# Kernel tuning notes

Hardware: AMD Instinct MI355X
Metric: run time of the kernel (lower is better)

Reference implementation:

```python
import jax, jax.numpy as jnp
import numpy as np

B, NPG, F, DEG = 512, 512, 255, 32   # graphs, nodes-per-graph, feat dim, avg degree
N = B * NPG
E = N * DEG
RATIO = 0.5
K = int(np.ceil(RATIO * NPG))        # nodes kept per graph (static)


def setup_inputs() -> dict:
    key = jax.random.key(0)
    k1, k2, k3, k4, k5 = jax.random.split(key, 5)
    out = jax.random.normal(k1, (N, F), jnp.float32)
    z = jax.random.randint(k2, (N,), 0, 101)  # z == 100 marks virtual nodes
    # random edges strictly within each graph (block-contiguous node ids)
    local = jax.random.randint(k3, (2, B, NPG * DEG), 0, NPG)
    offs = (jnp.arange(B) * NPG)[None, :, None]
    edge_index = (local + offs).reshape(2, E)
    batch = jnp.repeat(jnp.arange(B), NPG)
    W = jax.random.normal(k4, (F + 1, 1), jnp.float32) * (1.0 / np.sqrt(F + 1))
    b = jnp.zeros((1,), jnp.float32)
    edge_attr = jax.random.normal(k5, (E, 1), jnp.float32)  # carried but unused by SAGPool scoring
    return dict(out=out, z=z, edge_index=edge_index, batch=batch, W=W, b=b,
                edge_attr=edge_attr)


def gcn_score(x, edge_index, W, b):
    """GCNConv(F+1 -> 1) with self-loops and symmetric normalization."""
    n = x.shape[0]
    h = (x @ W)[:, 0]  # [N] since out_channels == 1
    row, col = edge_index[0], edge_index[1]
    loop = jnp.arange(n)
    row = jnp.concatenate([row, loop])
    col = jnp.concatenate([col, loop])
    deg = jax.ops.segment_sum(jnp.ones_like(col, x.dtype), col, num_segments=n)
    dinv = jnp.where(deg > 0, jax.lax.rsqrt(deg), 0.0)
    norm = dinv[row] * dinv[col]  # deg^-1/2 * deg^-1/2 per edge
    agg = jax.ops.segment_sum(norm * h[row], col, num_segments=n)
    return agg + b[0]


def reference(out, z, edge_index, batch, W, b, edge_attr):
    # concat real/virtual bit
    real = (z != 100).astype(out.dtype)[:, None]
    x = jnp.concatenate([out, real], axis=-1)          # [N, F+1]
    # SAGPooling: score nodes, tanh nonlinearity
    score = jnp.tanh(gcn_score(x, edge_index, W, b))   # [N]
    # per-graph top-k (uniform graph size -> static-shape top_k)
    sv, si = jax.lax.top_k(score.reshape(B, NPG), K)   # [B, K]
    perm = (si + (jnp.arange(B) * NPG)[:, None]).reshape(-1)  # global node ids
    xp = x[perm] * sv.reshape(-1)[:, None]             # gated selected nodes [B*K, F+1]
    # global_mean_pool over pooled batch (k nodes per graph)
    return xp.reshape(B, K, F + 1).mean(axis=1)        # [B, F+1]
```

## Files before the change

### kernel.cpp

```cpp
#include <hip/hip_runtime.h>
#include <math.h>

#define NPG     512
#define B_GR    512
#define FDIM    255
#define DEG     32
#define EPG     (NPG * DEG)
#define N_NODES (B_GR * NPG)
#define E_TOT   (N_NODES * DEG)
#define K_KEEP  256

#define CH_NODES 32
#define CH_F4    ((CH_NODES * FDIM) / 4)
#define NCHUNK   (NPG / CH_NODES)

__global__ __launch_bounds__(1024) void k_fused(const float* __restrict__ feat,
                                                const int*   __restrict__ z,
                                                const int*   __restrict__ ei,
                                                const float* __restrict__ W,
                                                const float* __restrict__ bias,
                                                float*       __restrict__ outp) {
    __shared__ __align__(16) char stagebuf[32768];
    __shared__ float Wl[256];
    __shared__ float h_l[NPG];
    __shared__ float dinv_l[NPG];
    __shared__ float agg[NPG];
    __shared__ float score[NPG];
    __shared__ float realb[NPG];
    __shared__ int   deg[NPG];
    __shared__ int   rank2[2][NPG];
    __shared__ int   selidx[K_KEEP];
    __shared__ float selsc[K_KEEP];
    __shared__ float red[3][256];
    __shared__ int   cnt;

    const int g     = blockIdx.x;
    const int tid   = threadIdx.x;
    const int nbase = g * NPG;

    if (tid < 256) Wl[tid] = W[tid];
    if (tid < NPG) {
        realb[tid] = (z[nbase + tid] != 100) ? 1.f : 0.f;
        deg[tid]   = 1;
        agg[tid]   = 0.f;
    }
    if (tid == 0) cnt = 0;
    __syncthreads();

    {
        float4*      stage4 = (float4*)stagebuf;
        const float* stage  = (const float*)stagebuf;
        const int    wave   = tid >> 6;
        const int    lane   = tid & 63;
        const float4* src   = (const float4*)(feat + (size_t)nbase * FDIM);

        for (int ch = 0; ch < NCHUNK; ++ch) {
            stage4[tid] = src[ch * CH_F4 + tid];
            const int idx2 = 1024 + tid;
            if (idx2 < CH_F4) stage4[idx2] = src[ch * CH_F4 + idx2];
            __syncthreads();
#pragma unroll
            for (int k = 0; k < 2; ++k) {
                const int node = wave * 2 + k;
                const float* row = stage + node * FDIM;
                float acc = (lane == 0) ? realb[ch * CH_NODES + node] * Wl[FDIM] : 0.f;
                acc = fmaf(row[lane],       Wl[lane],       acc);
                acc = fmaf(row[lane + 64],  Wl[lane + 64],  acc);
                acc = fmaf(row[lane + 128], Wl[lane + 128], acc);
                if (lane < 63)
                    acc = fmaf(row[lane + 192], Wl[lane + 192], acc);
#pragma unroll
                for (int off = 32; off; off >>= 1)
                    acc += __shfl_down(acc, off, 64);
                if (lane == 0) h_l[ch * CH_NODES + node] = acc;
            }
            __syncthreads();
        }
    }

    {
        ushort4*    cc4   = (ushort4*)stagebuf;
        const int4* colp4 = (const int4*)(ei + (size_t)E_TOT + (size_t)g * EPG);
        const int4* rowp4 = (const int4*)(ei + (size_t)g * EPG);

#pragma unroll
        for (int it = 0; it < 4; ++it) {
            const int  idx = it * 1024 + tid;
            const int4 c4  = colp4[idx];
            ushort4 u;
            u.x = (unsigned short)(c4.x - nbase);
            u.y = (unsigned short)(c4.y - nbase);
            u.z = (unsigned short)(c4.z - nbase);
            u.w = (unsigned short)(c4.w - nbase);
            cc4[idx] = u;
            atomicAdd(&deg[u.x], 1);
            atomicAdd(&deg[u.y], 1);
            atomicAdd(&deg[u.z], 1);
            atomicAdd(&deg[u.w], 1);
        }
        __syncthreads();

        if (tid < NPG)
            dinv_l[tid] = (float)(1.0 / sqrt((double)deg[tid]));
        __syncthreads();

#pragma unroll
        for (int it = 0; it < 4; ++it) {
            const int     idx = it * 1024 + tid;
            const int4    r4  = rowp4[idx];
            const ushort4 u   = cc4[idx];
            int r;
            r = r4.x - nbase; atomicAdd(&agg[u.x], dinv_l[r] * dinv_l[u.x] * h_l[r]);
            r = r4.y - nbase; atomicAdd(&agg[u.y], dinv_l[r] * dinv_l[u.y] * h_l[r]);
            r = r4.z - nbase; atomicAdd(&agg[u.z], dinv_l[r] * dinv_l[u.z] * h_l[r]);
            r = r4.w - nbase; atomicAdd(&agg[u.w], dinv_l[r] * dinv_l[u.w] * h_l[r]);
        }
        __syncthreads();
    }

    if (tid < NPG)
        score[tid] = tanhf(agg[tid] + dinv_l[tid] * dinv_l[tid] * h_l[tid] + bias[0]);
    __syncthreads();

    {
        const int   node = tid & (NPG - 1);
        const int   half = tid >> 9;
        const float sc   = score[node];
        const int   j0   = half * 256;
        int part = 0;
        for (int i = 0; i < 256; ++i) {
            const int   j  = j0 + i;
            const float sj = score[j];
            part += (sj > sc) || (sj == sc && j < node);
        }
        rank2[half][node] = part;
    }
    __syncthreads();

    if (tid < NPG) {
        const int rank = rank2[0][tid] + rank2[1][tid];
        if (rank < K_KEEP) {
            const int slot = atomicAdd(&cnt, 1);
            selidx[slot] = tid;
            selsc[slot]  = score[tid];
        }
    }
    __syncthreads();

    {
        const int f = tid & 255;
        const int q = tid >> 8;
        float acc = 0.f;
        if (f < FDIM) {
            const float* fb = feat + (size_t)nbase * FDIM + f;
#pragma unroll 8
            for (int s = q; s < K_KEEP; s += 4)
                acc = fmaf(selsc[s], fb[(size_t)selidx[s] * FDIM], acc);
        } else {
#pragma unroll 8
            for (int s = q; s < K_KEEP; s += 4)
                acc = fmaf(selsc[s], realb[selidx[s]], acc);
        }
        if (q) red[q - 1][f] = acc;
        __syncthreads();
        if (q == 0)
            outp[(size_t)g * 256 + f] =
                (acc + red[0][f] + red[1][f] + red[2][f]) * (1.f / K_KEEP);
    }
}

extern "C" void kernel_launch(void* const* d_in, const int* in_sizes, int n_in,
                              void* d_out, int out_size, void* d_ws, size_t ws_size,
                              hipStream_t stream) {
    const float* feat = (const float*)d_in[0];
    const int*   z    = (const int*)  d_in[1];
    const int*   ei   = (const int*)  d_in[2];
    const float* W    = (const float*)d_in[4];
    const float* bias = (const float*)d_in[5];
    float* outp = (float*)d_out;

    k_fused<<<B_GR, 1024, 0, stream>>>(feat, z, ei, W, bias, outp);
}
```

Before: 128.7 us.

## Double-buffer feature staging with direct global-to-LDS loads and vectorize rank scan

Replaces the register-staged feature copy with global_load_lds DMA into two LDS buffers of 16 nodes each, prefetching the next chunk while the current chunk's dot products run. One barrier per chunk replaces two, and the W values are hoisted into registers. The rank computation now reads scores as float4 with an unrolled loop. The trade-offs are more loop iterations with smaller chunks, and reliance on the 16-byte LDS DMA builtin and manual waitcnt handling.

```diff
diff --git a/kernel.cpp b/kernel.cpp
--- a/kernel.cpp
+++ b/kernel.cpp
@@ -10,9 +10,16 @@
 #define E_TOT   (N_NODES * DEG)
 #define K_KEEP  256
 
-#define CH_NODES 32
-#define CH_F4    ((CH_NODES * FDIM) / 4)
-#define NCHUNK   (NPG / CH_NODES)
+#define CH_NODES 16
+#define CH_FLOATS (CH_NODES * FDIM)
+#define CH_F4     (CH_FLOATS / 4)
+#define NCHUNK    (NPG / CH_NODES)
+
+__device__ __forceinline__ void lds_dma16(const void* g, void* l) {
+    __builtin_amdgcn_global_load_lds(
+        (const __attribute__((address_space(1))) unsigned int*)g,
+        (__attribute__((address_space(3))) unsigned int*)l, 16, 0, 0);
+}
 
 __global__ __launch_bounds__(1024) void k_fused(const float* __restrict__ feat,
                                                 const int*   __restrict__ z,
@@ -20,12 +27,12 @@
                                                 const float* __restrict__ W,
                                                 const float* __restrict__ bias,
                                                 float*       __restrict__ outp) {
-    __shared__ __align__(16) char stagebuf[32768];
-    __shared__ float Wl[256];
+    __shared__ __align__(16) float stage[2][CH_FLOATS];
+    __shared__ __align__(16) float Wl[256];
+    __shared__ __align__(16) float score[NPG];
     __shared__ float h_l[NPG];
     __shared__ float dinv_l[NPG];
     __shared__ float agg[NPG];
-    __shared__ float score[NPG];
     __shared__ float realb[NPG];
     __shared__ int   deg[NPG];
     __shared__ int   rank2[2][NPG];
@@ -37,6 +44,8 @@
     const int g     = blockIdx.x;
     const int tid   = threadIdx.x;
     const int nbase = g * NPG;
+    const int lane  = tid & 63;
+    const int wave  = tid >> 6;
 
     if (tid < 256) Wl[tid] = W[tid];
     if (tid < NPG) {
@@ -48,38 +57,47 @@
     __syncthreads();
 
     {
-        float4*      stage4 = (float4*)stagebuf;
-        const float* stage  = (const float*)stagebuf;
-        const int    wave   = tid >> 6;
-        const int    lane   = tid & 63;
-        const float4* src   = (const float4*)(feat + (size_t)nbase * FDIM);
+        const float w0   = Wl[lane];
+        const float w64  = Wl[lane + 64];
+        const float w128 = Wl[lane + 128];
+        const float w192 = (lane < 63) ? Wl[lane + 192] : 0.f;
+        const float w255 = Wl[FDIM];
+        const char* srcb = (const char*)(feat + (size_t)nbase * FDIM);
+
+        if (tid < CH_F4)
+            lds_dma16(srcb + (size_t)tid * 16, (char*)stage[0] + (size_t)tid * 16);
+        asm volatile("s_waitcnt vmcnt(0)" ::: "memory");
+        __builtin_amdgcn_s_barrier();
+        __builtin_amdgcn_sched_barrier(0);
 
         for (int ch = 0; ch < NCHUNK; ++ch) {
-            stage4[tid] = src[ch * CH_F4 + tid];
-            const int idx2 = 1024 + tid;
-            if (idx2 < CH_F4) stage4[idx2] = src[ch * CH_F4 + idx2];
-            __syncthreads();
+            const float* cur = stage[ch & 1];
+            float*       nxt = (float*)stage[(ch & 1) ^ 1];
+            if (ch + 1 < NCHUNK && tid < CH_F4)
+                lds_dma16(srcb + (size_t)(ch + 1) * 16320 + (size_t)tid * 16,
+                          (char*)nxt + (size_t)tid * 16);
+
+            const float* row = cur + wave * FDIM;
+            const float  rb  = realb[ch * CH_NODES + wave];
+            float acc = (lane == 0) ? rb * w255 : 0.f;
+            acc = fmaf(row[lane],       w0,   acc);
+            acc = fmaf(row[lane + 64],  w64,  acc);
+            acc = fmaf(row[lane + 128], w128, acc);
+            if (lane < 63)
+                acc = fmaf(row[lane + 192], w192, acc);
 #pragma unroll
-            for (int k = 0; k < 2; ++k) {
-                const int node = wave * 2 + k;
-                const float* row = stage + node * FDIM;
-                float acc = (lane == 0) ? realb[ch * CH_NODES + node] * Wl[FDIM] : 0.f;
-                acc = fmaf(row[lane],       Wl[lane],       acc);
-                acc = fmaf(row[lane + 64],  Wl[lane + 64],  acc);
-                acc = fmaf(row[lane + 128], Wl[lane + 128], acc);
-                if (lane < 63)
-                    acc = fmaf(row[lane + 192], Wl[lane + 192], acc);
-#pragma unroll
-                for (int off = 32; off; off >>= 1)
-                    acc += __shfl_down(acc, off, 64);
-                if (lane == 0) h_l[ch * CH_NODES + node] = acc;
-            }
-            __syncthreads();
-        }
-    }
-
-    {
-        ushort4*    cc4   = (ushort4*)stagebuf;
+            for (int off = 32; off; off >>= 1)
+                acc += __shfl_down(acc, off, 64);
+            if (lane == 0) h_l[ch * CH_NODES + wave] = acc;
+
+            asm volatile("s_waitcnt vmcnt(0)" ::: "memory");
+            __builtin_amdgcn_s_barrier();
+            __builtin_amdgcn_sched_barrier(0);
+        }
+    }
+
+    {
+        ushort4*    cc4   = (ushort4*)stage;
         const int4* colp4 = (const int4*)(ei + (size_t)E_TOT + (size_t)g * EPG);
         const int4* rowp4 = (const int4*)(ei + (size_t)g * EPG);
 
@@ -123,15 +141,19 @@
     __syncthreads();
 
     {
-        const int   node = tid & (NPG - 1);
-        const int   half = tid >> 9;
-        const float sc   = score[node];
-        const int   j0   = half * 256;
+        const int    node = tid & (NPG - 1);
+        const int    half = tid >> 9;
+        const float  sc   = score[node];
+        const float4* s4p = (const float4*)&score[half * 256];
         int part = 0;
-        for (int i = 0; i < 256; ++i) {
-            const int   j  = j0 + i;
-            const float sj = score[j];
-            part += (sj > sc) || (sj == sc && j < node);
+#pragma unroll 8
+        for (int i = 0; i < 64; ++i) {
+            const float4 s4 = s4p[i];
+            const int    j  = half * 256 + i * 4;
+            part += (s4.x > sc) || (s4.x == sc && (j + 0) < node);
+            part += (s4.y > sc) || (s4.y == sc && (j + 1) < node);
+            part += (s4.z > sc) || (s4.z == sc && (j + 2) < node);
+            part += (s4.w > sc) || (s4.w == sc && (j + 3) < node);
         }
         rank2[half][node] = part;
     }
```

Measured after the change: 118.4 us. -8.0%, faster.

## Split node projection into separate grid-stride kernel and simplify GCN aggregation

Applied to the files above, without the earlier changes.

Moves the feature-times-W projection out of the per-graph fused kernel into its own kernel. There each wave handles four nodes at a time through vectorized float4 loads and writes h to workspace. The scoring kernel folds the source dinv into h before edge aggregation and seeds agg with the self-loop, so each edge does a single atomic add with one multiply fewer. It also vectorizes the rank comparison loop and batches the gather loads for the final gated mean. The split removes LDS staging and the syncs in the projection loop. In exchange it adds a second launch and a round trip of h through global memory.

```diff
diff --git a/kernel.cpp b/kernel.cpp
--- a/kernel.cpp
+++ b/kernel.cpp
@@ -9,23 +9,88 @@
 #define N_NODES (B_GR * NPG)
 #define E_TOT   (N_NODES * DEG)
 #define K_KEEP  256
-
-#define CH_NODES 32
-#define CH_F4    ((CH_NODES * FDIM) / 4)
-#define NCHUNK   (NPG / CH_NODES)
-
-__global__ __launch_bounds__(1024) void k_fused(const float* __restrict__ feat,
+#define GRP_TOT (N_NODES / 4)
+
+__global__ __launch_bounds__(256) void k_proj(const float* __restrict__ feat,
+                                              const int*   __restrict__ z,
+                                              const float* __restrict__ W,
+                                              float*       __restrict__ h) {
+    __shared__ __align__(16) float Wx[1020];
+    __shared__ float w255s;
+
+    const int tid = threadIdx.x;
+    for (int k = tid; k < 1020; k += 256) Wx[k] = W[k % 255];
+    if (tid == 0) w255s = W[255];
+    __syncthreads();
+
+    const int lane = tid & 63;
+    const int wv   = tid >> 6;
+    const float4* W4 = (const float4*)Wx;
+    const float4* F4 = (const float4*)feat;
+    const int4*   Z4 = (const int4*)z;
+    float4*       H4 = (float4*)h;
+    const float w255 = w255s;
+    const bool  l63  = (lane == 63);
+
+    const float4 wf0 = W4[lane];
+    const float4 wf1 = W4[64 + lane];
+    const float4 wf2 = W4[128 + lane];
+    const float4 wf3 = l63 ? make_float4(0.f, 0.f, 0.f, 0.f) : W4[192 + lane];
+
+    const int nwaves = gridDim.x * 4;
+    for (int grp = blockIdx.x * 4 + wv; grp < GRP_TOT; grp += nwaves) {
+        const float4* src = F4 + (size_t)grp * 255;
+        const float4 a = src[lane];
+        const float4 b = src[64 + lane];
+        const float4 c = src[128 + lane];
+        const float4 d = l63 ? make_float4(0.f, 0.f, 0.f, 0.f) : src[192 + lane];
+
+        float acc0 = a.x * wf0.x + a.y * wf0.y + a.z * wf0.z;
+        const float p03 = a.w * wf0.w;
+        float acc1 = b.x * wf1.x + b.y * wf1.y;
+        const float p12 = b.z * wf1.z, p13 = b.w * wf1.w;
+        float acc2 = c.x * wf2.x;
+        const float p21 = c.y * wf2.y, p22 = c.z * wf2.z, p23 = c.w * wf2.w;
+        float acc3 = d.x * wf3.x + d.y * wf3.y + d.z * wf3.z + d.w * wf3.w;
+
+        const float q03 = p03;
+        const float q1  = p12 + p13;
+        const float q2  = p21 + p22 + p23;
+        acc0 += l63 ? 0.f : q03;
+        acc1 += l63 ? q03 : q1;
+        acc2 += l63 ? q1  : q2;
+        acc3 += l63 ? q2  : 0.f;
+
+#pragma unroll
+        for (int off = 32; off; off >>= 1) {
+            acc0 += __shfl_down(acc0, off, 64);
+            acc1 += __shfl_down(acc1, off, 64);
+            acc2 += __shfl_down(acc2, off, 64);
+            acc3 += __shfl_down(acc3, off, 64);
+        }
+        if (lane == 0) {
+            const int4 zz = Z4[grp];
+            float4 hv;
+            hv.x = acc0 + ((zz.x != 100) ? w255 : 0.f);
+            hv.y = acc1 + ((zz.y != 100) ? w255 : 0.f);
+            hv.z = acc2 + ((zz.z != 100) ? w255 : 0.f);
+            hv.w = acc3 + ((zz.w != 100) ? w255 : 0.f);
+            H4[grp] = hv;
+        }
+    }
+}
+
+__global__ __launch_bounds__(1024) void k_score(const float* __restrict__ feat,
                                                 const int*   __restrict__ z,
                                                 const int*   __restrict__ ei,
-                                                const float* __restrict__ W,
                                                 const float* __restrict__ bias,
+                                                const float* __restrict__ h,
                                                 float*       __restrict__ outp) {
-    __shared__ __align__(16) char stagebuf[32768];
-    __shared__ float Wl[256];
-    __shared__ float h_l[NPG];
+    __shared__ ushort4 cc4[EPG / 4];
+    __shared__ __align__(16) float score[NPG];
+    __shared__ float v_l[NPG];
     __shared__ float dinv_l[NPG];
     __shared__ float agg[NPG];
-    __shared__ float score[NPG];
     __shared__ float realb[NPG];
     __shared__ int   deg[NPG];
     __shared__ int   rank2[2][NPG];
@@ -38,100 +103,73 @@
     const int tid   = threadIdx.x;
     const int nbase = g * NPG;
 
-    if (tid < 256) Wl[tid] = W[tid];
+    const int4* colp4 = (const int4*)(ei + (size_t)E_TOT + (size_t)g * EPG);
+    const int4* rowp4 = (const int4*)(ei + (size_t)g * EPG);
+
     if (tid < NPG) {
+        v_l[tid]   = h[nbase + tid];
         realb[tid] = (z[nbase + tid] != 100) ? 1.f : 0.f;
         deg[tid]   = 1;
-        agg[tid]   = 0.f;
     }
     if (tid == 0) cnt = 0;
     __syncthreads();
 
+#pragma unroll
+    for (int it = 0; it < 4; ++it) {
+        const int  idx = it * 1024 + tid;
+        const int4 c4  = colp4[idx];
+        ushort4 u;
+        u.x = (unsigned short)(c4.x - nbase);
+        u.y = (unsigned short)(c4.y - nbase);
+        u.z = (unsigned short)(c4.z - nbase);
+        u.w = (unsigned short)(c4.w - nbase);
+        cc4[idx] = u;
+        atomicAdd(&deg[u.x], 1);
+        atomicAdd(&deg[u.y], 1);
+        atomicAdd(&deg[u.z], 1);
+        atomicAdd(&deg[u.w], 1);
+    }
+    __syncthreads();
+
+    if (tid < NPG) {
+        const float di = (float)(1.0 / sqrt((double)deg[tid]));
+        dinv_l[tid] = di;
+        const float v = di * v_l[tid];
+        v_l[tid] = v;
+        agg[tid] = v;
+    }
+    __syncthreads();
+
+#pragma unroll
+    for (int it = 0; it < 4; ++it) {
+        const int     idx = it * 1024 + tid;
+        const int4    r4  = rowp4[idx];
+        const ushort4 u   = cc4[idx];
+        atomicAdd(&agg[u.x], v_l[r4.x - nbase]);
+        atomicAdd(&agg[u.y], v_l[r4.y - nbase]);
+        atomicAdd(&agg[u.z], v_l[r4.z - nbase]);
+        atomicAdd(&agg[u.w], v_l[r4.w - nbase]);
+    }
+    __syncthreads();
+
+    if (tid < NPG)
+        score[tid] = tanhf(fmaf(agg[tid], dinv_l[tid], bias[0]));
+    __syncthreads();
+
     {
-        float4*      stage4 = (float4*)stagebuf;
-        const float* stage  = (const float*)stagebuf;
-        const int    wave   = tid >> 6;
-        const int    lane   = tid & 63;
-        const float4* src   = (const float4*)(feat + (size_t)nbase * FDIM);
-
-        for (int ch = 0; ch < NCHUNK; ++ch) {
-            stage4[tid] = src[ch * CH_F4 + tid];
-            const int idx2 = 1024 + tid;
-            if (idx2 < CH_F4) stage4[idx2] = src[ch * CH_F4 + idx2];
-            __syncthreads();
-#pragma unroll
-            for (int k = 0; k < 2; ++k) {
-                const int node = wave * 2 + k;
-                const float* row = stage + node * FDIM;
-                float acc = (lane == 0) ? realb[ch * CH_NODES + node] * Wl[FDIM] : 0.f;
-                acc = fmaf(row[lane],       Wl[lane],       acc);
-                acc = fmaf(row[lane + 64],  Wl[lane + 64],  acc);
-                acc = fmaf(row[lane + 128], Wl[lane + 128], acc);
-                if (lane < 63)
-                    acc = fmaf(row[lane + 192], Wl[lane + 192], acc);
-#pragma unroll
-                for (int off = 32; off; off >>= 1)
-                    acc += __shfl_down(acc, off, 64);
-                if (lane == 0) h_l[ch * CH_NODES + node] = acc;
-            }
-            __syncthreads();
-        }
-    }
-
-    {
-        ushort4*    cc4   = (ushort4*)stagebuf;
-        const int4* colp4 = (const int4*)(ei + (size_t)E_TOT + (size_t)g * EPG);
-        const int4* rowp4 = (const int4*)(ei + (size_t)g * EPG);
-
-#pragma unroll
-        for (int it = 0; it < 4; ++it) {
-            const int  idx = it * 1024 + tid;
-            const int4 c4  = colp4[idx];
-            ushort4 u;
-            u.x = (unsigned short)(c4.x - nbase);
-            u.y = (unsigned short)(c4.y - nbase);
-            u.z = (unsigned short)(c4.z - nbase);
-            u.w = (unsigned short)(c4.w - nbase);
-            cc4[idx] = u;
-            atomicAdd(&deg[u.x], 1);
-            atomicAdd(&deg[u.y], 1);
-            atomicAdd(&deg[u.z], 1);
-            atomicAdd(&deg[u.w], 1);
-        }
-        __syncthreads();
-
-        if (tid < NPG)
-            dinv_l[tid] = (float)(1.0 / sqrt((double)deg[tid]));
-        __syncthreads();
-
-#pragma unroll
-        for (int it = 0; it < 4; ++it) {
-            const int     idx = it * 1024 + tid;
-            const int4    r4  = rowp4[idx];
-            const ushort4 u   = cc4[idx];
-            int r;
-            r = r4.x - nbase; atomicAdd(&agg[u.x], dinv_l[r] * dinv_l[u.x] * h_l[r]);
-            r = r4.y - nbase; atomicAdd(&agg[u.y], dinv_l[r] * dinv_l[u.y] * h_l[r]);
-            r = r4.z - nbase; atomicAdd(&agg[u.z], dinv_l[r] * dinv_l[u.z] * h_l[r]);
-            r = r4.w - nbase; atomicAdd(&agg[u.w], dinv_l[r] * dinv_l[u.w] * h_l[r]);
-        }
-        __syncthreads();
-    }
-
-    if (tid < NPG)
-        score[tid] = tanhf(agg[tid] + dinv_l[tid] * dinv_l[tid] * h_l[tid] + bias[0]);
-    __syncthreads();
-
-    {
-        const int   node = tid & (NPG - 1);
-        const int   half = tid >> 9;
-        const float sc   = score[node];
-        const int   j0   = half * 256;
+        const int     node = tid & (NPG - 1);
+        const int     half = tid >> 9;
+        const float   sc   = score[node];
+        const float4* s4p  = (const float4*)&score[half * 256];
         int part = 0;
-        for (int i = 0; i < 256; ++i) {
-            const int   j  = j0 + i;
-            const float sj = score[j];
-            part += (sj > sc) || (sj == sc && j < node);
+#pragma unroll 8
+        for (int i = 0; i < 64; ++i) {
+            const float4 s4 = s4p[i];
+            const int    j  = half * 256 + i * 4;
+            part += (s4.x > sc) || (s4.x == sc && (j + 0) < node);
+            part += (s4.y > sc) || (s4.y == sc && (j + 1) < node);
+            part += (s4.z > sc) || (s4.z == sc && (j + 2) < node);
+            part += (s4.w > sc) || (s4.w == sc && (j + 3) < node);
         }
         rank2[half][node] = part;
     }
@@ -153,11 +191,22 @@
         float acc = 0.f;
         if (f < FDIM) {
             const float* fb = feat + (size_t)nbase * FDIM + f;
-#pragma unroll 8
-            for (int s = q; s < K_KEEP; s += 4)
-                acc = fmaf(selsc[s], fb[(size_t)selidx[s] * FDIM], acc);
+#pragma unroll
+            for (int k = 0; k < 64; k += 8) {
+                int   is[8]; float ss[8]; float tv[8];
+#pragma unroll
+                for (int j = 0; j < 8; ++j) {
+                    is[j] = selidx[q + 4 * (k + j)];
+                    ss[j] = selsc [q + 4 * (k + j)];
+                }
+#pragma unroll
+                for (int j = 0; j < 8; ++j)
+                    tv[j] = fb[(size_t)is[j] * FDIM];
+#pragma unroll
+                for (int j = 0; j < 8; ++j)
+                    acc = fmaf(ss[j], tv[j], acc);
+            }
         } else {
-#pragma unroll 8
             for (int s = q; s < K_KEEP; s += 4)
                 acc = fmaf(selsc[s], realb[selidx[s]], acc);
         }
@@ -178,6 +227,8 @@
     const float* W    = (const float*)d_in[4];
     const float* bias = (const float*)d_in[5];
     float* outp = (float*)d_out;
-
-    k_fused<<<B_GR, 1024, 0, stream>>>(feat, z, ei, W, bias, outp);
+    float* h    = (float*)d_ws;
+
+    k_proj <<<2048, 256,  0, stream>>>(feat, z, W, h);
+    k_score<<<B_GR, 1024, 0, stream>>>(feat, z, ei, bias, h, outp);
 }
```

Measured after the change: 125.3 us. 1.03x faster.
